# Kernel tuning notes

Measured on AMD Instinct MI355X. Metric: run time of the kernel, lower is better.

## Reference

```python
import jax, jax.numpy as jnp
import numpy as np

ACT_BITS = 8  # config.activation_bits
HIDDEN = 2048
INTERMEDIATE = 4096  # hidden * mlp_ratio (2.0), power of 2
EPS = 1e-5


def fwht(x):
    """Normalized fast Walsh-Hadamard transform along last axis (n = power of 2)."""
    shape = x.shape
    n = shape[-1]
    x = x.reshape(-1, n)
    h = 1
    while h < n:  # log2(n) fixed iterations, not a data-dim loop
        x = x.reshape(-1, n // (2 * h), 2, h)
        a, b = x[:, :, 0, :], x[:, :, 1, :]
        x = jnp.stack((a + b, a - b), axis=2).reshape(-1, n)
        h *= 2
    return (x * (1.0 / np.sqrt(n))).reshape(shape)


def _ste(x, q):
    # straight-through estimator: forward uses q, backward passes grad to x
    return x + jax.lax.stop_gradient(q - x)


def act_quant(x, bits):
    """Per-token absmax quantization to `bits` bits (BitNet a8 style), dequantized."""
    qb = float(2 ** (bits - 1) - 1)
    scale = qb / jnp.clip(jnp.max(jnp.abs(x), axis=-1, keepdims=True), EPS, None)
    q = jnp.clip(jnp.round(x * scale), -qb, qb) / scale
    return _ste(x, q)


def weight_quant(w):
    """Ternary absmean weight quantization (BitNet b1.58), dequantized."""
    scale = jnp.clip(jnp.mean(jnp.abs(w)), EPS, None)
    q = jnp.clip(jnp.round(w / scale), -1.0, 1.0) * scale
    return _ste(w, q)


def hbitlinear(x, w, bits):
    # H-BitLinear: Hadamard-rotate activations, quantize acts + weights, GEMM
    xq = act_quant(fwht(x), bits)
    wq = weight_quant(w)
    return jnp.einsum('bsd,fd->bsf', xq, wq)


def setup_inputs() -> dict:
    key = jax.random.key(0)
    k1, k2, k3 = jax.random.split(key, 3)
    hidden_states = jax.random.normal(k1, (4, 4096, HIDDEN), dtype=jnp.float32)
    w_up = jax.random.normal(k2, (INTERMEDIATE, HIDDEN), dtype=jnp.float32) * 0.02
    w_down = jax.random.normal(k3, (HIDDEN, INTERMEDIATE), dtype=jnp.float32) * 0.02
    return {"hidden_states": hidden_states, "w_up": w_up, "w_down": w_down}


def reference(hidden_states, w_up, w_down):
    h = hbitlinear(hidden_states, w_up, ACT_BITS)      # (B, S, intermediate)
    h = jnp.square(jax.nn.relu(h))                     # squared ReLU
    # dropout p=0.0 -> identity in eval/reference
    return hbitlinear(h, w_down, ACT_BITS)             # (B, S, hidden)
```

## Files before the change

### kernel.cpp

```cpp
#include <hip/hip_runtime.h>
#include <hip/hip_bf16.h>
#include <cstdint>
#include <cstddef>

#define HIDDEN 2048
#define INTER  4096
#define EPSQ   1e-5f

typedef int v4i __attribute__((ext_vector_type(4)));

__device__ __forceinline__ void async_ld16(const void* g, void* l) {
  __builtin_amdgcn_global_load_lds((const __attribute__((address_space(1))) void*)g,
                                   (__attribute__((address_space(3))) void*)l, 16, 0, 0);
}

__global__ void absmean_kernel(const float* __restrict__ w, size_t n4, double* __restrict__ out) {
  double s = 0.0;
  const float4* w4 = (const float4*)w;
  for (size_t i = blockIdx.x * (size_t)blockDim.x + threadIdx.x; i < n4;
       i += (size_t)gridDim.x * blockDim.x) {
    float4 v = w4[i];
    s += (double)fabsf(v.x) + (double)fabsf(v.y) + (double)fabsf(v.z) + (double)fabsf(v.w);
  }
  #pragma unroll
  for (int o = 32; o; o >>= 1) s += __shfl_down(s, o);
  __shared__ double red[4];
  if ((threadIdx.x & 63) == 0) red[threadIdx.x >> 6] = s;
  __syncthreads();
  if (threadIdx.x == 0) atomicAdd(out, red[0] + red[1] + red[2] + red[3]);
}

__global__ void quantw_kernel(const float* __restrict__ w, size_t n4,
                              const double* __restrict__ sum, double invcnt,
                              int8_t* __restrict__ q) {
  const float scale = (float)fmax(sum[0] * invcnt, (double)EPSQ);
  const float4* w4 = (const float4*)w;
  char4* q4 = (char4*)q;
  for (size_t i = blockIdx.x * (size_t)blockDim.x + threadIdx.x; i < n4;
       i += (size_t)gridDim.x * blockDim.x) {
    float4 v = w4[i];
    char4 c;
    c.x = (signed char)fmaxf(-1.f, fminf(1.f, rintf(v.x / scale)));
    c.y = (signed char)fmaxf(-1.f, fminf(1.f, rintf(v.y / scale)));
    c.z = (signed char)fmaxf(-1.f, fminf(1.f, rintf(v.z / scale)));
    c.w = (signed char)fmaxf(-1.f, fminf(1.f, rintf(v.w / scale)));
    q4[i] = c;
  }
}

template <int LOGN>
__global__ void fwht_quant_kernel(const float* __restrict__ X, int8_t* __restrict__ Q,
                                  float* __restrict__ invs) {
  constexpr int N = 1 << LOGN;
  constexpr int E = N / 256;
  __shared__ float s[N];
  __shared__ float red[4];
  const int tid = threadIdx.x;
  const size_t t = blockIdx.x;
  const float4* xt = (const float4*)(X + t * (size_t)N);
  #pragma unroll
  for (int u = 0; u < N / 1024; ++u) ((float4*)s)[tid + u * 256] = xt[tid + u * 256];
  __syncthreads();
  #pragma unroll
  for (int st = 0; st < LOGN; ++st) {
    const int h = 1 << st;
    #pragma unroll
    for (int u = 0; u < N / 512; ++u) {
      const int p = tid + u * 256;
      const int i = ((p >> st) << (st + 1)) | (p & (h - 1));
      const float a = s[i], b = s[i + h];
      s[i] = a + b;
      s[i + h] = a - b;
    }
    __syncthreads();
  }
  const float c = (LOGN == 11) ? 0.022097086912079608f : 0.015625f;
  float r[E];
  float mx = 0.f;
  #pragma unroll
  for (int e = 0; e < E; ++e) {
    float v = s[tid * E + e] * c;
    r[e] = v;
    mx = fmaxf(mx, fabsf(v));
  }
  #pragma unroll
  for (int o = 32; o; o >>= 1) mx = fmaxf(mx, __shfl_down(mx, o));
  if ((tid & 63) == 0) red[tid >> 6] = mx;
  __syncthreads();
  mx = fmaxf(fmaxf(red[0], red[1]), fmaxf(red[2], red[3]));
  mx = fmaxf(mx, EPSQ);
  const float scale = 127.0f / mx;
  if (tid == 0) invs[t] = mx / 127.0f;
  alignas(16) int8_t qv[E];
  #pragma unroll
  for (int e = 0; e < E; ++e) {
    float q = rintf(r[e] * scale);
    q = fmaxf(-127.f, fminf(127.f, q));
    qv[e] = (int8_t)q;
  }
  if constexpr (E == 8)
    *(int2*)(Q + t * (size_t)N + tid * E) = *(const int2*)qv;
  else
    *(int4*)(Q + t * (size_t)N + tid * E) = *(const int4*)qv;
}

template <bool RELU2>
__global__ void gemm_i8_kernel(const int8_t* __restrict__ A, const int8_t* __restrict__ B,
                               float* __restrict__ C, const float* __restrict__ invs,
                               const double* __restrict__ wsum, double invcnt,
                               int N, int K) {
  __shared__ int8_t As[128 * 64];
  __shared__ int8_t Bs[128 * 64];
  const int tid = threadIdx.x;
  const int lane = tid & 63, wave = tid >> 6;
  const int wr = wave >> 1, wc = wave & 1;
  const int m0 = blockIdx.y * 128, n0 = blockIdx.x * 128;

  v4i acc[4][4] = {};

  const int row = tid >> 2;
  const int colb = (tid & 3) * 16;
  const int8_t* gA0 = A + (size_t)(m0 + row) * K + colb;
  const int8_t* gA1 = A + (size_t)(m0 + row + 64) * K + colb;
  const int8_t* gB0 = B + (size_t)(n0 + row) * K + colb;
  const int8_t* gB1 = B + (size_t)(n0 + row + 64) * K + colb;
  int8_t* lA0 = As + tid * 16;
  int8_t* lA1 = As + 4096 + tid * 16;
  int8_t* lB0 = Bs + tid * 16;
  int8_t* lB1 = Bs + 4096 + tid * 16;

  const int afrag = (wr * 64 + (lane & 15)) * 64 + (lane >> 4) * 16;
  const int bfrag = (wc * 64 + (lane & 15)) * 64 + (lane >> 4) * 16;

  for (int k0 = 0; k0 < K; k0 += 64) {
    async_ld16(gA0 + k0, lA0);
    async_ld16(gA1 + k0, lA1);
    async_ld16(gB0 + k0, lB0);
    async_ld16(gB1 + k0, lB1);
    __syncthreads();
    v4i a[4], b[4];
    #pragma unroll
    for (int mt = 0; mt < 4; ++mt) a[mt] = *(const v4i*)(As + afrag + mt * 1024);
    #pragma unroll
    for (int nt = 0; nt < 4; ++nt) b[nt] = *(const v4i*)(Bs + bfrag + nt * 1024);
    #pragma unroll
    for (int mt = 0; mt < 4; ++mt)
      #pragma unroll
      for (int nt = 0; nt < 4; ++nt)
        acc[mt][nt] = __builtin_amdgcn_mfma_i32_16x16x64_i8(a[mt], b[nt], acc[mt][nt], 0, 0, 0);
    __syncthreads();
  }

  const float wscale = (float)fmax(wsum[0] * invcnt, (double)EPSQ);
  #pragma unroll
  for (int mt = 0; mt < 4; ++mt) {
    const int trow = m0 + wr * 64 + mt * 16 + (lane >> 4) * 4;
    float fr[4];
    #pragma unroll
    for (int r = 0; r < 4; ++r) fr[r] = wscale * invs[trow + r];
    const int col = n0 + wc * 64 + (lane & 15);
    #pragma unroll
    for (int nt = 0; nt < 4; ++nt) {
      #pragma unroll
      for (int r = 0; r < 4; ++r) {
        float v = (float)acc[mt][nt][r] * fr[r];
        if (RELU2) v = v > 0.f ? v * v : 0.f;
        C[(size_t)(trow + r) * N + (col + nt * 16)] = v;
      }
    }
  }
}

extern "C" void kernel_launch(void* const* d_in, const int* in_sizes, int n_in,
                              void* d_out, int out_size, void* d_ws, size_t ws_size,
                              hipStream_t stream) {
  const float* x      = (const float*)d_in[0];
  const float* w_up   = (const float*)d_in[1];
  const float* w_down = (const float*)d_in[2];
  float* out = (float*)d_out;

  const int T = in_sizes[0] / HIDDEN;
  const size_t WN = (size_t)INTER * HIDDEN;

  char* ws = (char*)d_ws;
  double* sums   = (double*)ws;
  float* invs1   = (float*)(ws + 256);
  float* invs2   = (float*)(ws + 256 + 65536);
  int8_t* wq_up  = (int8_t*)(ws + 131328);
  int8_t* wq_dn  = wq_up + WN;
  int8_t* a8_1   = wq_dn + WN;
  int8_t* a8_2   = a8_1 + (size_t)T * HIDDEN;
  float*  h      = (float*)(a8_2 + (size_t)T * INTER);

  const double invcnt = 1.0 / (double)WN;

  hipMemsetAsync(sums, 0, 256, stream);
  absmean_kernel<<<1024, 256, 0, stream>>>(w_up, WN / 4, sums + 0);
  absmean_kernel<<<1024, 256, 0, stream>>>(w_down, WN / 4, sums + 1);
  quantw_kernel<<<2048, 256, 0, stream>>>(w_up, WN / 4, sums + 0, invcnt, wq_up);
  quantw_kernel<<<2048, 256, 0, stream>>>(w_down, WN / 4, sums + 1, invcnt, wq_dn);

  fwht_quant_kernel<11><<<T, 256, 0, stream>>>(x, a8_1, invs1);
  gemm_i8_kernel<true><<<dim3(INTER / 128, T / 128), 256, 0, stream>>>(
      a8_1, wq_up, h, invs1, sums + 0, invcnt, INTER, HIDDEN);
  fwht_quant_kernel<12><<<T, 256, 0, stream>>>(h, a8_2, invs2);
  gemm_i8_kernel<false><<<dim3(HIDDEN / 128, T / 128), 256, 0, stream>>>(
      a8_2, wq_dn, out, invs2, sums + 1, invcnt, HIDDEN, INTER);
}
```

Measured before the change: 776.7 us.

## Do FWHT per-wave in registers with shuffles; store intermediate in fp16

The Hadamard-quantize kernel now gives each token to one wavefront. It does the in-thread butterflies in registers and the cross-lane stages with xor shuffles, which removes the shared-memory stages and the block barriers between them. The first GEMM now writes the squared-ReLU intermediate as fp16 instead of fp32, halving the traffic for that tensor on both the write and the read by the second FWHT. The risks are fp16 overflow or precision loss in the squared activations, which could change the quantized values, and much higher register pressure (E=64 floats per thread for the 4096-wide transform).

Result: faster. 696.5 us (-10.3%).

```diff
diff --git a/kernel.cpp b/kernel.cpp
--- a/kernel.cpp
+++ b/kernel.cpp
@@ -1,5 +1,5 @@
 #include <hip/hip_runtime.h>
-#include <hip/hip_bf16.h>
+#include <hip/hip_fp16.h>
 #include <cstdint>
 #include <cstddef>
 
@@ -48,65 +48,81 @@
   }
 }
 
-template <int LOGN>
-__global__ void fwht_quant_kernel(const float* __restrict__ X, int8_t* __restrict__ Q,
-                                  float* __restrict__ invs) {
+template <int LOGN, bool HALF_IN>
+__global__ void __launch_bounds__(256) fwht_quant_kernel(const void* __restrict__ Xv,
+                                                         int8_t* __restrict__ Q,
+                                                         float* __restrict__ invs) {
   constexpr int N = 1 << LOGN;
-  constexpr int E = N / 256;
-  __shared__ float s[N];
-  __shared__ float red[4];
-  const int tid = threadIdx.x;
-  const size_t t = blockIdx.x;
-  const float4* xt = (const float4*)(X + t * (size_t)N);
-  #pragma unroll
-  for (int u = 0; u < N / 1024; ++u) ((float4*)s)[tid + u * 256] = xt[tid + u * 256];
-  __syncthreads();
-  #pragma unroll
-  for (int st = 0; st < LOGN; ++st) {
-    const int h = 1 << st;
-    #pragma unroll
-    for (int u = 0; u < N / 512; ++u) {
-      const int p = tid + u * 256;
-      const int i = ((p >> st) << (st + 1)) | (p & (h - 1));
-      const float a = s[i], b = s[i + h];
-      s[i] = a + b;
-      s[i + h] = a - b;
-    }
-    __syncthreads();
-  }
-  const float c = (LOGN == 11) ? 0.022097086912079608f : 0.015625f;
+  constexpr int E = N / 64;
+  const int lane = threadIdx.x & 63;
+  const size_t t = (size_t)blockIdx.x * 4 + (threadIdx.x >> 6);
+
   float r[E];
+  if constexpr (HALF_IN) {
+    const int4* xp = (const int4*)((const __half*)Xv + t * (size_t)N + lane * E);
+    #pragma unroll
+    for (int u = 0; u < E / 8; ++u) {
+      alignas(16) __half hb[8];
+      *(int4*)hb = xp[u];
+      #pragma unroll
+      for (int j = 0; j < 8; ++j) r[u * 8 + j] = __half2float(hb[j]);
+    }
+  } else {
+    const float4* xp = (const float4*)((const float*)Xv + t * (size_t)N + lane * E);
+    #pragma unroll
+    for (int u = 0; u < E / 4; ++u) {
+      float4 v = xp[u];
+      r[u * 4 + 0] = v.x; r[u * 4 + 1] = v.y; r[u * 4 + 2] = v.z; r[u * 4 + 3] = v.w;
+    }
+  }
+
+  #pragma unroll
+  for (int m = 1; m < E; m <<= 1) {
+    #pragma unroll
+    for (int e = 0; e < E; ++e) {
+      if (!(e & m)) {
+        float a = r[e], b = r[e | m];
+        r[e] = a + b;
+        r[e | m] = a - b;
+      }
+    }
+  }
+  #pragma unroll
+  for (int m = 1; m < 64; m <<= 1) {
+    const float sgn = (lane & m) ? -1.f : 1.f;
+    #pragma unroll
+    for (int e = 0; e < E; ++e) {
+      float w = __shfl_xor(r[e], m, 64);
+      r[e] = fmaf(r[e], sgn, w);
+    }
+  }
+
   float mx = 0.f;
   #pragma unroll
+  for (int e = 0; e < E; ++e) mx = fmaxf(mx, fabsf(r[e]));
+  #pragma unroll
+  for (int m = 1; m < 64; m <<= 1) mx = fmaxf(mx, __shfl_xor(mx, m, 64));
+
+  constexpr float c = (LOGN == 11) ? 0.022097086912079608f : 0.015625f;
+  mx = fmaxf(mx * c, EPSQ);
+  const float sc = 127.0f * c / mx;
+  if (lane == 0) invs[t] = mx * (1.0f / 127.0f);
+
+  alignas(16) int8_t qv[E];
+  #pragma unroll
   for (int e = 0; e < E; ++e) {
-    float v = s[tid * E + e] * c;
-    r[e] = v;
-    mx = fmaxf(mx, fabsf(v));
-  }
-  #pragma unroll
-  for (int o = 32; o; o >>= 1) mx = fmaxf(mx, __shfl_down(mx, o));
-  if ((tid & 63) == 0) red[tid >> 6] = mx;
-  __syncthreads();
-  mx = fmaxf(fmaxf(red[0], red[1]), fmaxf(red[2], red[3]));
-  mx = fmaxf(mx, EPSQ);
-  const float scale = 127.0f / mx;
-  if (tid == 0) invs[t] = mx / 127.0f;
-  alignas(16) int8_t qv[E];
-  #pragma unroll
-  for (int e = 0; e < E; ++e) {
-    float q = rintf(r[e] * scale);
+    float q = rintf(r[e] * sc);
     q = fmaxf(-127.f, fminf(127.f, q));
     qv[e] = (int8_t)q;
   }
-  if constexpr (E == 8)
-    *(int2*)(Q + t * (size_t)N + tid * E) = *(const int2*)qv;
-  else
-    *(int4*)(Q + t * (size_t)N + tid * E) = *(const int4*)qv;
-}
-
-template <bool RELU2>
+  int8_t* qp = Q + t * (size_t)N + lane * E;
+  #pragma unroll
+  for (int u = 0; u < E / 16; ++u) ((int4*)qp)[u] = ((const int4*)qv)[u];
+}
+
+template <bool RELU2, typename TOUT>
 __global__ void gemm_i8_kernel(const int8_t* __restrict__ A, const int8_t* __restrict__ B,
-                               float* __restrict__ C, const float* __restrict__ invs,
+                               TOUT* __restrict__ C, const float* __restrict__ invs,
                                const double* __restrict__ wsum, double invcnt,
                                int N, int K) {
   __shared__ int8_t As[128 * 64];
@@ -165,7 +181,10 @@
       for (int r = 0; r < 4; ++r) {
         float v = (float)acc[mt][nt][r] * fr[r];
         if (RELU2) v = v > 0.f ? v * v : 0.f;
-        C[(size_t)(trow + r) * N + (col + nt * 16)] = v;
+        if constexpr (sizeof(TOUT) == 2)
+          C[(size_t)(trow + r) * N + (col + nt * 16)] = __float2half(v);
+        else
+          C[(size_t)(trow + r) * N + (col + nt * 16)] = v;
       }
     }
   }
@@ -190,7 +209,7 @@
   int8_t* wq_dn  = wq_up + WN;
   int8_t* a8_1   = wq_dn + WN;
   int8_t* a8_2   = a8_1 + (size_t)T * HIDDEN;
-  float*  h      = (float*)(a8_2 + (size_t)T * INTER);
+  __half* h      = (__half*)(a8_2 + (size_t)T * INTER);
 
   const double invcnt = 1.0 / (double)WN;
 
@@ -200,10 +219,10 @@
   quantw_kernel<<<2048, 256, 0, stream>>>(w_up, WN / 4, sums + 0, invcnt, wq_up);
   quantw_kernel<<<2048, 256, 0, stream>>>(w_down, WN / 4, sums + 1, invcnt, wq_dn);
 
-  fwht_quant_kernel<11><<<T, 256, 0, stream>>>(x, a8_1, invs1);
-  gemm_i8_kernel<true><<<dim3(INTER / 128, T / 128), 256, 0, stream>>>(
+  fwht_quant_kernel<11, false><<<T / 4, 256, 0, stream>>>(x, a8_1, invs1);
+  gemm_i8_kernel<true, __half><<<dim3(INTER / 128, T / 128), 256, 0, stream>>>(
       a8_1, wq_up, h, invs1, sums + 0, invcnt, INTER, HIDDEN);
-  fwht_quant_kernel<12><<<T, 256, 0, stream>>>(h, a8_2, invs2);
-  gemm_i8_kernel<false><<<dim3(HIDDEN / 128, T / 128), 256, 0, stream>>>(
+  fwht_quant_kernel<12, true><<<T / 4, 256, 0, stream>>>(h, a8_2, invs2);
+  gemm_i8_kernel<false, float><<<dim3(HIDDEN / 128, T / 128), 256, 0, stream>>>(
       a8_2, wq_dn, out, invs2, sums + 1, invcnt, HIDDEN, INTER);
 }
```
